# Optimization experiments

Hardware: AMD Instinct MI355X
Metric: run time of the kernel (lower is better)

Reference implementation:

```python
import jax, jax.numpy as jnp
import numpy as np
from functools import partial

N_NODES = 100000
N_EDGES = 1600000
N_LABEL = 200000
D = 128


def _add_self_loops(edge_index, edge_weight, num_nodes):
    # PyG GCNConv default: add self loops with fill_value = 1.0
    loops = jnp.arange(num_nodes, dtype=edge_index.dtype)
    src = jnp.concatenate([edge_index[0], loops])
    dst = jnp.concatenate([edge_index[1], loops])
    ew = jnp.concatenate([edge_weight, jnp.ones((num_nodes,), edge_weight.dtype)])
    return src, dst, ew


def _gcn_norm(src, dst, ew, num_nodes):
    # symmetric normalization: D^-1/2 A D^-1/2, degrees over target index
    deg = jax.ops.segment_sum(ew, dst, num_segments=num_nodes)
    dinv = jnp.where(deg > 0, jax.lax.rsqrt(deg), 0.0)
    return dinv[src] * ew * dinv[dst]


def _gcn_conv(x, W, b, src, dst, norm, num_nodes):
    h = x @ W                      # [N, D] small GEMM
    msg = h[src] * norm[:, None]   # gather + scale, [E+N, D]
    out = jax.ops.segment_sum(msg, dst, num_segments=num_nodes)
    return out + b


def setup_inputs() -> dict:
    key = jax.random.key(0)
    ks = jax.random.split(key, 10)
    s = 1.0 / np.sqrt(D)
    return {
        "x": jax.random.normal(ks[0], (N_NODES, D), jnp.float32),
        "edge_index": jax.random.randint(ks[1], (2, N_EDGES), 0, N_NODES, jnp.int64),
        "edge_weight": jax.random.uniform(ks[2], (N_EDGES,), jnp.float32),
        "edge_label_index": jax.random.randint(ks[3], (2, N_LABEL), 0, N_NODES, jnp.int64),
        "W1": jax.random.uniform(ks[4], (D, D), jnp.float32, -s, s),
        "b1": jnp.zeros((D,), jnp.float32),
        "W2": jax.random.uniform(ks[5], (D, D), jnp.float32, -s, s),
        "b2": jnp.zeros((D,), jnp.float32),
        "lin_W": jax.random.uniform(ks[6], (D, D), jnp.float32, -s, s),
        "lin_b": jax.random.uniform(ks[7], (D,), jnp.float32, -s, s),
    }


def reference(x, edge_index, edge_weight, edge_label_index, W1, b1, W2, b2, lin_W, lin_b):
    n = x.shape[0]
    src, dst, ew = _add_self_loops(edge_index, edge_weight, n)
    norm = _gcn_norm(src, dst, ew, n)
    out = jax.nn.relu(_gcn_conv(x, W1, b1, src, dst, norm, n))
    out = jax.nn.relu(_gcn_conv(out, W2, b2, src, dst, norm, n))
    had = out[edge_label_index[0]] * out[edge_label_index[1]]  # [EL, D]
    # lin then sum over features == had @ lin_W @ 1 + sum(lin_b)
    return jnp.sum(had @ lin_W + lin_b, axis=-1)
```

## Files before the change

### kernel.cpp

```cpp
#include <hip/hip_runtime.h>

#define N_NODES 100000
#define N_EDGES 1600000
#define N_LABEL 200000
#define D 128

#define SCAN_BLOCKS ((N_NODES + 255) / 256)

typedef __attribute__((ext_vector_type(8))) short short8;
typedef __attribute__((ext_vector_type(4))) float f32x4;

static __device__ __forceinline__ unsigned short f2bf(float f) {
    unsigned u = __float_as_uint(f);
    u += 0x7fffu + ((u >> 16) & 1u);
    return (unsigned short)(u >> 16);
}
static __device__ __forceinline__ float bf2f_lo(unsigned p) {
    return __uint_as_float(p << 16);
}
static __device__ __forceinline__ float bf2f_hi(unsigned p) {
    return __uint_as_float(p & 0xffff0000u);
}

__global__ void k_prep(const float* __restrict__ linW, const float* __restrict__ linb,
                       float* __restrict__ wv, float* __restrict__ cval) {
    int t = threadIdx.x;
    float s = 0.f;
    for (int j = 0; j < D; ++j) s += linW[t * D + j];
    wv[t] = s;
    __shared__ float red[128];
    red[t] = linb[t];
    __syncthreads();
    for (int st = 64; st > 0; st >>= 1) {
        if (t < st) red[t] += red[t + st];
        __syncthreads();
    }
    if (t == 0) *cval = red[0];
}

__global__ void k_prepw(const float* __restrict__ W, unsigned short* __restrict__ Wt) {
    int i = blockIdx.x * 256 + threadIdx.x;
    if (i < D * D) {
        int k = i >> 7, n = i & 127;
        Wt[n * D + k] = f2bf(W[i]);
    }
}

__global__ void k_init(int* __restrict__ cnt8) {
    int i = blockIdx.x * 256 + threadIdx.x;
    if (i < 8 * N_NODES) cnt8[i] = 0;
}

__global__ void k_count(const int* __restrict__ ei, int* __restrict__ cnt8,
                        int* __restrict__ rank) {
    int e = blockIdx.x * 256 + threadIdx.x;
    int p = blockIdx.x & 7;
    if (e < N_EDGES) rank[e] = atomicAdd(&cnt8[p * N_NODES + ei[N_EDGES + e]], 1);
}

__global__ void k_scan1(const int* __restrict__ cnt8, int* __restrict__ offs,
                        int* __restrict__ bsum) {
    __shared__ int sm[256];
    int tid = threadIdx.x;
    int i = blockIdx.x * 256 + tid;
    int v = 0;
    if (i < N_NODES) {
#pragma unroll
        for (int q = 0; q < 8; ++q) v += cnt8[q * N_NODES + i];
    }
    sm[tid] = v;
    __syncthreads();
    for (int st = 1; st < 256; st <<= 1) {
        int add = (tid >= st) ? sm[tid - st] : 0;
        __syncthreads();
        sm[tid] += add;
        __syncthreads();
    }
    if (i < N_NODES) offs[i] = sm[tid] - v;
    if (tid == 255) bsum[blockIdx.x] = sm[255];
}

__global__ void k_scan2(int* __restrict__ bsum) {
    __shared__ int sm[512];
    int tid = threadIdx.x;
    int v = (tid < SCAN_BLOCKS) ? bsum[tid] : 0;
    sm[tid] = v;
    __syncthreads();
    for (int st = 1; st < 512; st <<= 1) {
        int add = (tid >= st) ? sm[tid - st] : 0;
        __syncthreads();
        sm[tid] += add;
        __syncthreads();
    }
    if (tid < SCAN_BLOCKS) bsum[tid] = sm[tid] - v;
}

__global__ void k_scan3(int* __restrict__ offs, const int* __restrict__ bsum,
                        const int* __restrict__ cnt8, int* __restrict__ pofs) {
    int i = blockIdx.x * 256 + threadIdx.x;
    if (i < N_NODES) {
        int base = offs[i] + bsum[i >> 8];
        offs[i] = base;
#pragma unroll
        for (int q = 0; q < 8; ++q) {
            pofs[q * N_NODES + i] = base;
            base += cnt8[q * N_NODES + i];
        }
    }
    if (i == 0) offs[N_NODES] = N_EDGES;
}

__global__ void k_scatter(const int* __restrict__ ei, const float* __restrict__ ew,
                          const int* __restrict__ pofs, const int* __restrict__ rank,
                          int2* __restrict__ csr) {
    int e = blockIdx.x * 256 + threadIdx.x;
    int p = blockIdx.x & 7;
    if (e < N_EDGES) {
        int d = ei[N_EDGES + e];
        int pos = pofs[p * N_NODES + d] + rank[e];
        csr[pos] = make_int2(ei[e] << 6, __float_as_int(ew[e]));
    }
}

__global__ void k_degdinv(const int* __restrict__ offs, const int2* __restrict__ csr,
                          float* __restrict__ dinv) {
    int i = blockIdx.x * 256 + threadIdx.x;
    if (i < N_NODES) {
        int p0 = offs[i], p1 = offs[i + 1];
        float s = 1.0f;
        for (int p = p0; p < p1; ++p) s += __int_as_float(csr[p].y);
        dinv[i] = rsqrtf(s);
    }
}

template <bool IN_F32>
__global__ __launch_bounds__(256) void k_gemm(const void* __restrict__ INp,
                                              const unsigned short* __restrict__ Wt,
                                              const float* __restrict__ dinv,
                                              unsigned short* __restrict__ H) {
    __shared__ unsigned short xs[64 * 128];
    __shared__ unsigned short wts[128 * 128];
    int tid = threadIdx.x;
    int rowBase = blockIdx.x * 64;

#pragma unroll
    for (int i = 0; i < 4; ++i) {
        int idx = tid + i * 256;
        int r = idx >> 4;
        int kc = (idx & 15) << 3;
        int gr = rowBase + r;
        uint4 pk = make_uint4(0, 0, 0, 0);
        if (gr < N_NODES) {
            if (IN_F32) {
                const float* X = (const float*)INp;
                float4 v0 = *(const float4*)&X[(size_t)gr * D + kc];
                float4 v1 = *(const float4*)&X[(size_t)gr * D + kc + 4];
                pk.x = (unsigned)f2bf(v0.x) | ((unsigned)f2bf(v0.y) << 16);
                pk.y = (unsigned)f2bf(v0.z) | ((unsigned)f2bf(v0.w) << 16);
                pk.z = (unsigned)f2bf(v1.x) | ((unsigned)f2bf(v1.y) << 16);
                pk.w = (unsigned)f2bf(v1.z) | ((unsigned)f2bf(v1.w) << 16);
            } else {
                pk = *(const uint4*)&((const unsigned short*)INp)[(size_t)gr * D + kc];
            }
        }
        *(uint4*)&xs[(r * D + kc) ^ ((r & 7) << 3)] = pk;
    }
#pragma unroll
    for (int i = 0; i < 8; ++i) {
        int idx = tid + i * 256;
        int n = idx >> 4;
        int kc = (idx & 15) << 3;
        uint4 pk = *(const uint4*)&Wt[n * D + kc];
        *(uint4*)&wts[(n * D + kc) ^ ((n & 7) << 3)] = pk;
    }
    __syncthreads();

    int lane = tid & 63;
    int wrow = (tid >> 6) * 16;
    int l15 = lane & 15;
    int l4 = (lane >> 4) << 2;

    f32x4 acc[8] = {};
    union FragU { short8 v; uint2 u2[2]; };

#pragma unroll
    for (int kk = 0; kk < 4; ++kk) {
        int kb = kk * 32 + l4;
        int m = wrow + l15;
        FragU a;
        a.u2[0] = *(uint2*)&xs[(m * D + kb) ^ ((m & 7) << 3)];
        a.u2[1] = *(uint2*)&xs[(m * D + kb + 16) ^ ((m & 7) << 3)];
#pragma unroll
        for (int ct = 0; ct < 8; ++ct) {
            int n = ct * 16 + l15;
            FragU b;
            b.u2[0] = *(uint2*)&wts[(n * D + kb) ^ ((n & 7) << 3)];
            b.u2[1] = *(uint2*)&wts[(n * D + kb + 16) ^ ((n & 7) << 3)];
            acc[ct] = __builtin_amdgcn_mfma_f32_16x16x32_bf16(a.v, b.v, acc[ct], 0, 0, 0);
        }
    }

    int rloc = wrow + l4;
    float dn[4];
#pragma unroll
    for (int r = 0; r < 4; ++r) {
        int gr = rowBase + rloc + r;
        dn[r] = (gr < N_NODES) ? dinv[gr] : 0.f;
    }
#pragma unroll
    for (int ct = 0; ct < 8; ++ct) {
#pragma unroll
        for (int r = 0; r < 4; ++r) {
            int gr = rowBase + rloc + r;
            if (gr < N_NODES)
                H[(size_t)gr * D + ct * 16 + l15] = f2bf(acc[ct][r] * dn[r]);
        }
    }
}

__global__ __launch_bounds__(256) void k_agg(const unsigned* __restrict__ h,
                                             const float* __restrict__ dinv,
                                             const int* __restrict__ offs,
                                             const int2* __restrict__ csr,
                                             const float* __restrict__ bias,
                                             unsigned* __restrict__ out) {
    int wid = threadIdx.x >> 6;
    int lane = threadIdx.x & 63;
    int node = blockIdx.x * 4 + wid;
    if (node >= N_NODES) return;

    int eh = lane >> 5;
    int fl = lane & 31;

    float a0 = 0.f, a1 = 0.f, a2 = 0.f, a3 = 0.f;
    int p0 = offs[node], p1 = offs[node + 1];

    for (int p = p0; p < p1; p += 32) {
        int2 cc[16];
        float ww[16];
#pragma unroll
        for (int k = 0; k < 16; ++k) {
            int pe = p + (k << 1) + eh;
            bool v = pe < p1;
            cc[k] = csr[v ? pe : p0];
            ww[k] = v ? __int_as_float(cc[k].y) : 0.f;
        }
        uint2 hh[16];
#pragma unroll
        for (int k = 0; k < 16; ++k)
            hh[k] = *(const uint2*)&h[(size_t)(unsigned)cc[k].x + fl * 2];
#pragma unroll
        for (int k = 0; k < 16; ++k) {
            a0 += ww[k] * bf2f_lo(hh[k].x);
            a1 += ww[k] * bf2f_hi(hh[k].x);
            a2 += ww[k] * bf2f_lo(hh[k].y);
            a3 += ww[k] * bf2f_hi(hh[k].y);
        }
    }

    a0 += __shfl_xor(a0, 32, 64);
    a1 += __shfl_xor(a1, 32, 64);
    a2 += __shfl_xor(a2, 32, 64);
    a3 += __shfl_xor(a3, 32, 64);

    if (eh == 0) {
        uint2 sv = *(const uint2*)&h[(size_t)node * 64 + fl * 2];
        a0 += bf2f_lo(sv.x);
        a1 += bf2f_hi(sv.x);
        a2 += bf2f_lo(sv.y);
        a3 += bf2f_hi(sv.y);
        float dn = dinv[node];
        float4 bb = *(const float4*)&bias[fl * 4];
        a0 = fmaxf(a0 * dn + bb.x, 0.f);
        a1 = fmaxf(a1 * dn + bb.y, 0.f);
        a2 = fmaxf(a2 * dn + bb.z, 0.f);
        a3 = fmaxf(a3 * dn + bb.w, 0.f);
        uint2 o;
        o.x = (unsigned)f2bf(a0) | ((unsigned)f2bf(a1) << 16);
        o.y = (unsigned)f2bf(a2) | ((unsigned)f2bf(a3) << 16);
        *(uint2*)&out[(size_t)node * 64 + fl * 2] = o;
    }
}

__global__ void k_final(const int* __restrict__ eli, const unsigned* __restrict__ o2,
                        const float* __restrict__ wv, const float* __restrict__ cval,
                        float* __restrict__ res) {
    unsigned g = blockIdx.x * 256 + threadIdx.x;
    int l = g >> 6;
    int t = g & 63;
    if (l < N_LABEL) {
        int a = eli[l];
        int b = eli[N_LABEL + l];
        unsigned ua = o2[(size_t)a * 64 + t];
        unsigned ub = o2[(size_t)b * 64 + t];
        float2 w2 = *(const float2*)&wv[t * 2];
        float s = bf2f_lo(ua) * bf2f_lo(ub) * w2.x + bf2f_hi(ua) * bf2f_hi(ub) * w2.y;
#pragma unroll
        for (int st = 32; st > 0; st >>= 1) s += __shfl_down(s, st, 64);
        if (t == 0) res[l] = s + *cval;
    }
}

extern "C" void kernel_launch(void* const* d_in, const int* in_sizes, int n_in,
                              void* d_out, int out_size, void* d_ws, size_t ws_size,
                              hipStream_t stream) {
    const float* x    = (const float*)d_in[0];
    const int*   ei   = (const int*)d_in[1];
    const float* ew   = (const float*)d_in[2];
    const int*   eli  = (const int*)d_in[3];
    const float* W1   = (const float*)d_in[4];
    const float* b1   = (const float*)d_in[5];
    const float* W2   = (const float*)d_in[6];
    const float* b2   = (const float*)d_in[7];
    const float* linW = (const float*)d_in[8];
    const float* linb = (const float*)d_in[9];
    float* res = (float*)d_out;

    float*          ws    = (float*)d_ws;
    float*          dinv  = ws;
    int*            offs  = (int*)(dinv + N_NODES);
    int*            bsum  = offs + N_NODES + 4;
    int*            cnt8  = bsum + 512;
    int*            pofs  = cnt8 + 8 * N_NODES;
    int2*           csr   = (int2*)(pofs + 8 * N_NODES);
    unsigned*       h_bf  = (unsigned*)(csr + N_EDGES);
    unsigned*       agg   = h_bf + (size_t)N_NODES * 64;
    unsigned*       out2  = agg + (size_t)N_NODES * 64;
    float*          wv    = (float*)(out2 + (size_t)N_NODES * 64);
    float*          cval  = wv + D;
    unsigned short* w1t   = (unsigned short*)(cval + 1);
    unsigned short* w2t   = w1t + D * D;
    int*            rank  = (int*)agg;

    k_prep<<<1, 128, 0, stream>>>(linW, linb, wv, cval);
    k_prepw<<<64, 256, 0, stream>>>(W1, w1t);
    k_prepw<<<64, 256, 0, stream>>>(W2, w2t);

    k_init<<<(8 * N_NODES + 255) / 256, 256, 0, stream>>>(cnt8);
    k_count<<<(N_EDGES + 255) / 256, 256, 0, stream>>>(ei, cnt8, rank);
    k_scan1<<<SCAN_BLOCKS, 256, 0, stream>>>(cnt8, offs, bsum);
    k_scan2<<<1, 512, 0, stream>>>(bsum);
    k_scan3<<<SCAN_BLOCKS, 256, 0, stream>>>(offs, bsum, cnt8, pofs);
    k_scatter<<<(N_EDGES + 255) / 256, 256, 0, stream>>>(ei, ew, pofs, rank, csr);
    k_degdinv<<<(N_NODES + 255) / 256, 256, 0, stream>>>(offs, csr, dinv);

    const int GB = (N_NODES + 63) / 64;

    k_gemm<true><<<GB, 256, 0, stream>>>(x, w1t, dinv, (unsigned short*)h_bf);
    k_agg<<<(N_NODES + 3) / 4, 256, 0, stream>>>(h_bf, dinv, offs, csr, b1, agg);

    k_gemm<false><<<GB, 256, 0, stream>>>(agg, w2t, dinv, (unsigned short*)h_bf);
    k_agg<<<(N_NODES + 3) / 4, 256, 0, stream>>>(h_bf, dinv, offs, csr, b2, out2);

    k_final<<<(N_LABEL * 64 + 255) / 256, 256, 0, stream>>>(eli, out2, wv, cval, res);
}
```

Before: 378.9 us.

## Merge prep kernels, add nontemporal loads/stores, shrink agg batch to 16 edges

Fuses the three weight-prep kernels into one launch. Adds nontemporal loads and stores for streaming edge arrays, the rank buffer and CSR records, and stores each CSR record as a single 64-bit word. Halves the per-iteration edge batch in the aggregation kernel from 32 to 16, which cuts registers and wasted padded loads for low-degree nodes but exposes less memory-level parallelism per wave. Nontemporal stores to csr may hurt, since that array is re-read soon by degdinv and agg.

```diff
diff --git a/kernel.cpp b/kernel.cpp
--- a/kernel.cpp
+++ b/kernel.cpp
@@ -22,27 +22,35 @@
     return __uint_as_float(p & 0xffff0000u);
 }
 
-__global__ void k_prep(const float* __restrict__ linW, const float* __restrict__ linb,
-                       float* __restrict__ wv, float* __restrict__ cval) {
-    int t = threadIdx.x;
-    float s = 0.f;
-    for (int j = 0; j < D; ++j) s += linW[t * D + j];
-    wv[t] = s;
-    __shared__ float red[128];
-    red[t] = linb[t];
-    __syncthreads();
-    for (int st = 64; st > 0; st >>= 1) {
-        if (t < st) red[t] += red[t + st];
-        __syncthreads();
-    }
-    if (t == 0) *cval = red[0];
-}
-
-__global__ void k_prepw(const float* __restrict__ W, unsigned short* __restrict__ Wt) {
-    int i = blockIdx.x * 256 + threadIdx.x;
-    if (i < D * D) {
+__global__ void k_prepall(const float* __restrict__ linW, const float* __restrict__ linb,
+                          const float* __restrict__ W1, const float* __restrict__ W2,
+                          float* __restrict__ wv, float* __restrict__ cval,
+                          unsigned short* __restrict__ w1t,
+                          unsigned short* __restrict__ w2t) {
+    int b = blockIdx.x;
+    if (b == 0) {
+        int t = threadIdx.x;
+        if (t < 128) {
+            float s = 0.f;
+            for (int j = 0; j < D; ++j) s += linW[t * D + j];
+            wv[t] = s;
+        }
+        __shared__ float red[128];
+        if (t < 128) red[t] = linb[t];
+        __syncthreads();
+        for (int st = 64; st > 0; st >>= 1) {
+            if (t < st) red[t] += red[t + st];
+            __syncthreads();
+        }
+        if (t == 0) *cval = red[0];
+    } else if (b <= 64) {
+        int i = (b - 1) * 256 + threadIdx.x;
         int k = i >> 7, n = i & 127;
-        Wt[n * D + k] = f2bf(W[i]);
+        w1t[n * D + k] = f2bf(W1[i]);
+    } else {
+        int i = (b - 65) * 256 + threadIdx.x;
+        int k = i >> 7, n = i & 127;
+        w2t[n * D + k] = f2bf(W2[i]);
     }
 }
 
@@ -55,7 +63,11 @@
                         int* __restrict__ rank) {
     int e = blockIdx.x * 256 + threadIdx.x;
     int p = blockIdx.x & 7;
-    if (e < N_EDGES) rank[e] = atomicAdd(&cnt8[p * N_NODES + ei[N_EDGES + e]], 1);
+    if (e < N_EDGES) {
+        int d = __builtin_nontemporal_load(&ei[N_EDGES + e]);
+        int r = atomicAdd(&cnt8[p * N_NODES + d], 1);
+        __builtin_nontemporal_store(r, &rank[e]);
+    }
 }
 
 __global__ void k_scan1(const int* __restrict__ cnt8, int* __restrict__ offs,
@@ -112,23 +124,31 @@
 
 __global__ void k_scatter(const int* __restrict__ ei, const float* __restrict__ ew,
                           const int* __restrict__ pofs, const int* __restrict__ rank,
-                          int2* __restrict__ csr) {
+                          long long* __restrict__ csr) {
     int e = blockIdx.x * 256 + threadIdx.x;
     int p = blockIdx.x & 7;
     if (e < N_EDGES) {
-        int d = ei[N_EDGES + e];
-        int pos = pofs[p * N_NODES + d] + rank[e];
-        csr[pos] = make_int2(ei[e] << 6, __float_as_int(ew[e]));
-    }
-}
-
-__global__ void k_degdinv(const int* __restrict__ offs, const int2* __restrict__ csr,
+        int s = __builtin_nontemporal_load(&ei[e]);
+        int d = __builtin_nontemporal_load(&ei[N_EDGES + e]);
+        float w = __builtin_nontemporal_load(&ew[e]);
+        int r = __builtin_nontemporal_load(&rank[e]);
+        int pos = pofs[p * N_NODES + d] + r;
+        long long rec = (long long)(unsigned)(s << 6) |
+                        ((long long)(unsigned)__float_as_int(w) << 32);
+        __builtin_nontemporal_store(rec, &csr[pos]);
+    }
+}
+
+__global__ void k_degdinv(const int* __restrict__ offs, const long long* __restrict__ csr,
                           float* __restrict__ dinv) {
     int i = blockIdx.x * 256 + threadIdx.x;
     if (i < N_NODES) {
         int p0 = offs[i], p1 = offs[i + 1];
         float s = 1.0f;
-        for (int p = p0; p < p1; ++p) s += __int_as_float(csr[p].y);
+        for (int p = p0; p < p1; ++p) {
+            long long rec = __builtin_nontemporal_load(&csr[p]);
+            s += __int_as_float((int)(rec >> 32));
+        }
         dinv[i] = rsqrtf(s);
     }
 }
@@ -221,7 +241,7 @@
 __global__ __launch_bounds__(256) void k_agg(const unsigned* __restrict__ h,
                                              const float* __restrict__ dinv,
                                              const int* __restrict__ offs,
-                                             const int2* __restrict__ csr,
+                                             const long long* __restrict__ csr,
                                              const float* __restrict__ bias,
                                              unsigned* __restrict__ out) {
     int wid = threadIdx.x >> 6;
@@ -235,22 +255,23 @@
     float a0 = 0.f, a1 = 0.f, a2 = 0.f, a3 = 0.f;
     int p0 = offs[node], p1 = offs[node + 1];
 
-    for (int p = p0; p < p1; p += 32) {
-        int2 cc[16];
-        float ww[16];
-#pragma unroll
-        for (int k = 0; k < 16; ++k) {
+    for (int p = p0; p < p1; p += 16) {
+        unsigned so[8];
+        float ww[8];
+#pragma unroll
+        for (int k = 0; k < 8; ++k) {
             int pe = p + (k << 1) + eh;
             bool v = pe < p1;
-            cc[k] = csr[v ? pe : p0];
-            ww[k] = v ? __int_as_float(cc[k].y) : 0.f;
-        }
-        uint2 hh[16];
-#pragma unroll
-        for (int k = 0; k < 16; ++k)
-            hh[k] = *(const uint2*)&h[(size_t)(unsigned)cc[k].x + fl * 2];
-#pragma unroll
-        for (int k = 0; k < 16; ++k) {
+            long long rec = __builtin_nontemporal_load(&csr[v ? pe : p0]);
+            so[k] = (unsigned)(int)rec;
+            ww[k] = v ? __int_as_float((int)(rec >> 32)) : 0.f;
+        }
+        uint2 hh[8];
+#pragma unroll
+        for (int k = 0; k < 8; ++k)
+            hh[k] = *(const uint2*)&h[(size_t)so[k] + fl * 2];
+#pragma unroll
+        for (int k = 0; k < 8; ++k) {
             a0 += ww[k] * bf2f_lo(hh[k].x);
             a1 += ww[k] * bf2f_hi(hh[k].x);
             a2 += ww[k] * bf2f_lo(hh[k].y);
@@ -322,7 +343,7 @@
     int*            bsum  = offs + N_NODES + 4;
     int*            cnt8  = bsum + 512;
     int*            pofs  = cnt8 + 8 * N_NODES;
-    int2*           csr   = (int2*)(pofs + 8 * N_NODES);
+    long long*      csr   = (long long*)(pofs + 8 * N_NODES);
     unsigned*       h_bf  = (unsigned*)(csr + N_EDGES);
     unsigned*       agg   = h_bf + (size_t)N_NODES * 64;
     unsigned*       out2  = agg + (size_t)N_NODES * 64;
@@ -332,9 +353,7 @@
     unsigned short* w2t   = w1t + D * D;
     int*            rank  = (int*)agg;
 
-    k_prep<<<1, 128, 0, stream>>>(linW, linb, wv, cval);
-    k_prepw<<<64, 256, 0, stream>>>(W1, w1t);
-    k_prepw<<<64, 256, 0, stream>>>(W2, w2t);
+    k_prepall<<<129, 256, 0, stream>>>(linW, linb, W1, W2, wv, cval, w1t, w2t);
 
     k_init<<<(8 * N_NODES + 255) / 256, 256, 0, stream>>>(cnt8);
     k_count<<<(N_EDGES + 255) / 256, 256, 0, stream>>>(ei, cnt8, rank);
```

After: 433.2 us. 1.14x slower.
